# Optimization experiments

Hardware: AMD Instinct MI355X
Metric: run time of the kernel (lower is better)

Reference implementation:

```python
import jax, jax.numpy as jnp
import numpy as np

NX, NY = 8192, 8192
FX, FY = 1024, 1024
EMB, EMB_OUT = 512, 512


def setup_inputs() -> dict:
    key = jax.random.key(0)
    ks = jax.random.split(key, 8)
    s = lambda f: 1.0 / np.sqrt(f)
    return {
        "x": jax.random.normal(ks[0], (NX, FX), jnp.float32),
        "y": jax.random.normal(ks[1], (NY, FY), jnp.float32),
        "Wx": jax.random.uniform(ks[2], (FX, EMB), jnp.float32, -s(FX), s(FX)),
        "bx": jax.random.uniform(ks[3], (EMB,), jnp.float32, -s(FX), s(FX)),
        "Wy": jax.random.uniform(ks[4], (FY, EMB), jnp.float32, -s(FY), s(FY)),
        "by": jax.random.uniform(ks[5], (EMB,), jnp.float32, -s(FY), s(FY)),
        "Wg": jax.random.uniform(ks[6], (EMB, EMB_OUT), jnp.float32, -s(EMB), s(EMB)),
        "bg": jax.random.uniform(ks[7], (EMB_OUT,), jnp.float32, -s(EMB), s(EMB)),
    }


def reference(x, y, Wx, bx, Wy, by, Wg, bg):
    # Linear projections: [Nx, emb], [Ny, emb]
    xp = x @ Wx + bx
    yp = y @ Wy + by
    # Pairwise affinity (Dice-coefficient style normalization)
    A_ = xp @ yp.T                              # [Nx, Ny]
    Dcol = jnp.sum(xp * xp, axis=1)[:, None]    # ||x_i||^2, diag of xp@xp.T
    Drow = jnp.sum(yp * yp, axis=1)[None, :]    # ||y_j||^2, diag of yp@yp.T
    A = 2.0 * A_ / (Dcol + Drow)                # [Nx, Ny]
    # Weighted aggregation over x nodes, then ReLU MLP
    gwf = A.T @ xp                              # [Ny, emb]
    return jax.nn.relu(gwf @ Wg + bg)           # [Ny, emb_out]
```

## Files before the change

### kernel.cpp

```cpp
#include <hip/hip_runtime.h>
#include <hip/hip_bf16.h>


typedef __attribute__((ext_vector_type(8))) short bf16x8;
typedef __attribute__((ext_vector_type(4))) short bf16x4;
typedef __attribute__((ext_vector_type(4))) float f32x4;

__device__ __forceinline__ short f2b(float f) {
    unsigned int u = __builtin_bit_cast(unsigned int, f);
    unsigned int r = (u + 0x7fffu + ((u >> 16) & 1u)) >> 16;
    return (short)r;
}
__device__ __forceinline__ float b2f(short s) {
    unsigned int u = ((unsigned int)(unsigned short)s) << 16;
    return __builtin_bit_cast(float, u);
}

__device__ __forceinline__ void cp16(const void* g, void* l) {
    __builtin_amdgcn_global_load_lds(
        (const __attribute__((address_space(1))) void*)g,
        (__attribute__((address_space(3))) void*)l, 16, 0, 0);
}

template<int N>
__device__ __forceinline__ void waitvm() {
    if constexpr (N == 0)      asm volatile("s_waitcnt vmcnt(0)" ::: "memory");
    else if constexpr (N == 4) asm volatile("s_waitcnt vmcnt(4)" ::: "memory");
    else if constexpr (N == 6) asm volatile("s_waitcnt vmcnt(6)" ::: "memory");
    else if constexpr (N == 8) asm volatile("s_waitcnt vmcnt(8)" ::: "memory");
    else static_assert(N == 0, "unsupported vmcnt literal");
}

constexpr int EPI_XP = 0;
constexpr int EPI_BF = 1;
constexpr int EPI_AT = 2;

template<int EPI, int TM, int TN, int WVN>
__device__ __forceinline__ void gemm_core(
    const short* __restrict__ A, int lda,
    const short* __restrict__ Bt, int ldb,
    int N, int K, int bm, int bn, int kbase,
    const float* __restrict__ bias,
    short* __restrict__ outb,
    float* __restrict__ Dacc,
    const float* __restrict__ Drow, const float* __restrict__ Dcol)
{
    constexpr int WN  = WVN;
    constexpr int WM  = 4 / WN;
    constexpr int FRN = TN / WN / 16;
    constexpr int FRM = TM / WM / 16;
    __shared__ __align__(16) short As[TM * 32];
    __shared__ __align__(16) short Bs[TN * 32];

    const int tid  = threadIdx.x;
    const int wave = tid >> 6;
    const int lane = tid & 63;
    const int quad = lane >> 4;
    const int l15  = lane & 15;
    const int wn   = (wave % WN) * (FRN * 16);
    const int wm   = (wave / WN) * (FRM * 16);

    f32x4 acc[FRM][FRN];
#pragma unroll
    for (int i = 0; i < FRM; i++)
#pragma unroll
        for (int j = 0; j < FRN; j++) acc[i][j] = f32x4{0.f, 0.f, 0.f, 0.f};

    for (int k0 = kbase; k0 < kbase + K; k0 += 32) {
#pragma unroll
        for (int s = 0; s < TM / 64; s++) {
            const int seg = tid + 256 * s;
            const int row = seg >> 2, c8 = seg & 3;
            const int gg  = c8 ^ (row & 3);
            cp16(&A[(size_t)(bm + row) * lda + k0 + gg * 8], &As[seg * 8]);
        }
#pragma unroll
        for (int s = 0; s < TN / 64; s++) {
            const int seg = tid + 256 * s;
            const int row = seg >> 2, c8 = seg & 3;
            const int gg  = c8 ^ (row & 3);
            cp16(&Bt[(size_t)(bn + row) * ldb + k0 + gg * 8], &Bs[seg * 8]);
        }
        __syncthreads();

        bf16x8 a[FRM], b[FRN];
#pragma unroll
        for (int i = 0; i < FRM; i++) {
            const int row = wm + i * 16 + l15;
            a[i] = *(const bf16x8*)&As[row * 32 + ((quad ^ (row & 3)) << 3)];
        }
#pragma unroll
        for (int j = 0; j < FRN; j++) {
            const int row = wn + j * 16 + l15;
            b[j] = *(const bf16x8*)&Bs[row * 32 + ((quad ^ (row & 3)) << 3)];
        }
#pragma unroll
        for (int i = 0; i < FRM; i++)
#pragma unroll
            for (int j = 0; j < FRN; j++)
                acc[i][j] = __builtin_amdgcn_mfma_f32_16x16x32_bf16(a[i], b[j], acc[i][j], 0, 0, 0);
        __syncthreads();
    }

#pragma unroll
    for (int im = 0; im < FRM; ++im) {
#pragma unroll
        for (int r = 0; r < 4; ++r) {
            const int gm = bm + wm + im * 16 + quad * 4 + r;
            if (EPI == EPI_XP) {
                float s = 0.f;
#pragma unroll
                for (int jn = 0; jn < FRN; ++jn) {
                    const int gn = bn + wn + jn * 16 + l15;
                    const float v = acc[im][jn][r] + bias[gn];
                    outb[(size_t)gm * N + gn] = f2b(v);
                    s += v * v;
                }
#pragma unroll
                for (int m = 1; m < 16; m <<= 1) s += __shfl_xor(s, m, 64);
                if (l15 == 0) atomicAdd(&Dacc[gm], s);
            } else {
#pragma unroll
                for (int jn = 0; jn < FRN; ++jn) {
                    const int gn = bn + wn + jn * 16 + l15;
                    outb[(size_t)gm * N + gn] = f2b(acc[im][jn][r]);
                }
            }
        }
    }
}

template<int EPI, int TM, int TN, int RING>
__device__ __forceinline__ void gemm_deep(
    const short* __restrict__ A, int lda,
    const short* __restrict__ Bt, int ldb,
    int N, int K, int bm, int bn, int kbase,
    short* __restrict__ outb,
    const float* __restrict__ Drow, const float* __restrict__ Dcol)
{
    constexpr int FRM = TM / 32;
    constexpr int FRN = TN / 32;
    constexpr int CPA = TM * 4 / 256;
    constexpr int CPB = TN * 4 / 256;
    constexpr int CPT = CPA + CPB;
    __shared__ __align__(16) short As[RING][TM * 32];
    __shared__ __align__(16) short Bs[RING][TN * 32];

    const int tid  = threadIdx.x;
    const int wave = tid >> 6;
    const int lane = tid & 63;
    const int quad = lane >> 4;
    const int l15  = lane & 15;
    const int wm   = (wave >> 1) * (FRM * 16);
    const int wn   = (wave & 1) * (FRN * 16);
    const int nk   = K / 32;

    f32x4 acc[FRM][FRN];
#pragma unroll
    for (int i = 0; i < FRM; i++)
#pragma unroll
        for (int j = 0; j < FRN; j++) acc[i][j] = f32x4{0.f, 0.f, 0.f, 0.f};

    auto stage = [&](int slot, int t) {
        const int k0 = kbase + t * 32;
#pragma unroll
        for (int s = 0; s < CPA; s++) {
            const int seg = tid + 256 * s;
            const int row = seg >> 2, c8 = seg & 3;
            const int gg  = c8 ^ (row & 3);
            cp16(&A[(size_t)(bm + row) * lda + k0 + gg * 8], &As[slot][seg * 8]);
        }
#pragma unroll
        for (int s = 0; s < CPB; s++) {
            const int seg = tid + 256 * s;
            const int row = seg >> 2, c8 = seg & 3;
            const int gg  = c8 ^ (row & 3);
            cp16(&Bt[(size_t)(bn + row) * ldb + k0 + gg * 8], &Bs[slot][seg * 8]);
        }
    };

#pragma unroll
    for (int p = 0; p < RING - 1; ++p) stage(p, p);

    int cur = 0, prv = RING - 1;
    for (int t = 0; t < nk; ++t) {
        if constexpr (RING == 3) {
            if (t + 1 < nk) waitvm<CPT>(); else waitvm<0>();
        } else {
            if (t + 2 < nk)      waitvm<2 * CPT>();
            else if (t + 1 < nk) waitvm<CPT>();
            else                 waitvm<0>();
        }
        __builtin_amdgcn_s_barrier();
        if (t + RING - 1 < nk) stage(prv, t + RING - 1);

        bf16x8 a[FRM], b[FRN];
#pragma unroll
        for (int i = 0; i < FRM; i++) {
            const int row = wm + i * 16 + l15;
            a[i] = *(const bf16x8*)&As[cur][row * 32 + ((quad ^ (row & 3)) << 3)];
        }
#pragma unroll
        for (int j = 0; j < FRN; j++) {
            const int row = wn + j * 16 + l15;
            b[j] = *(const bf16x8*)&Bs[cur][row * 32 + ((quad ^ (row & 3)) << 3)];
        }
        __builtin_amdgcn_s_setprio(1);
#pragma unroll
        for (int i = 0; i < FRM; i++)
#pragma unroll
            for (int j = 0; j < FRN; j++)
                acc[i][j] = __builtin_amdgcn_mfma_f32_16x16x32_bf16(a[i], b[j], acc[i][j], 0, 0, 0);
        __builtin_amdgcn_s_setprio(0);
        asm volatile("s_waitcnt lgkmcnt(0)" ::: "memory");
        prv = cur;
        cur = (cur + 1 == RING) ? 0 : cur + 1;
    }

    if (EPI == EPI_AT) {
        float dcol[FRN];
#pragma unroll
        for (int jn = 0; jn < FRN; ++jn) dcol[jn] = Dcol[bn + wn + jn * 16 + l15];
#pragma unroll
        for (int im = 0; im < FRM; ++im) {
#pragma unroll
            for (int r = 0; r < 4; ++r) {
                const int gm = bm + wm + im * 16 + quad * 4 + r;
                const float dy = Drow[gm];
#pragma unroll
                for (int jn = 0; jn < FRN; ++jn) {
                    const int gn = bn + wn + jn * 16 + l15;
                    const float v = 2.f * acc[im][jn][r] * __builtin_amdgcn_rcpf(dcol[jn] + dy);
                    outb[(size_t)gm * N + gn] = f2b(v);
                }
            }
        }
    } else {
#pragma unroll
        for (int im = 0; im < FRM; ++im) {
#pragma unroll
            for (int r = 0; r < 4; ++r) {
                const int gm = bm + wm + im * 16 + quad * 4 + r;
#pragma unroll
                for (int jn = 0; jn < FRN; ++jn) {
                    const int gn = bn + wn + jn * 16 + l15;
                    outb[(size_t)gm * N + gn] = f2b(acc[im][jn][r]);
                }
            }
        }
    }
}

__global__ __launch_bounds__(256)
void k_proj(const short* __restrict__ A, const short* __restrict__ Bt,
            const float* __restrict__ bias, short* __restrict__ outb,
            float* __restrict__ Dacc)
{
    gemm_core<EPI_XP, 64, 128, 2>(A, 1024, Bt, 1024, 512, 1024,
                                  blockIdx.y * 64, blockIdx.x * 128, 0,
                                  bias, outb, Dacc, nullptr, nullptr);
}

__global__ __launch_bounds__(256)
void k_zT(const short* __restrict__ WgT, const short* __restrict__ xpb,
          short* __restrict__ zT)
{
    gemm_core<EPI_BF, 64, 128, 2>(WgT, 512, xpb, 512, 8192, 512,
                                  blockIdx.y * 64, blockIdx.x * 128, 0,
                                  nullptr, zT, nullptr, nullptr, nullptr);
}

__global__ __launch_bounds__(256, 2)
void k_aff(const short* __restrict__ ypb, const short* __restrict__ xpb,
           short* __restrict__ At, const float* __restrict__ Dy,
           const float* __restrict__ Dx)
{
    const int flat = blockIdx.x;
    const int xcd = flat & 7;
    const int q   = flat >> 3;
    const int by  = xcd * 4 + (q & 3);
    const int bx  = q >> 2;
    gemm_deep<EPI_AT, 256, 128, 3>(ypb, 512, xpb, 512, 8192, 512,
                                   by * 256, bx * 128, 0, At, Dy, Dx);
}

__global__ __launch_bounds__(256, 2)
void k_agg(const short* __restrict__ At, const short* __restrict__ zT,
           short* __restrict__ p0, short* __restrict__ p1)
{
    const int flat = blockIdx.x;
    const int xcd = flat & 7;
    const int q   = flat >> 3;
    const int g   = xcd * 16 + (q >> 2);
    const int bm  = (g >> 1) * 128;
    const int z   = g & 1;
    const int bn  = (q & 3) * 128;
    short* outb = z ? p1 : p0;
    gemm_deep<EPI_BF, 128, 128, 4>(At, 8192, zT, 8192, 512, 4096,
                                   bm, bn, z * 4096, outb, nullptr, nullptr);
}

__global__ __launch_bounds__(256)
void k_fin(const short* __restrict__ p0, const short* __restrict__ p1,
           const float* __restrict__ bg, float* __restrict__ out)
{
    const int idx = (blockIdx.x * 256 + threadIdx.x) * 8;
    const int col = idx & 511;
    const bf16x8 a = *(const bf16x8*)&p0[idx];
    const bf16x8 b = *(const bf16x8*)&p1[idx];
    const f32x4 g0 = *(const f32x4*)&bg[col];
    const f32x4 g1 = *(const f32x4*)&bg[col + 4];
    f32x4 o0, o1;
#pragma unroll
    for (int e = 0; e < 4; ++e) {
        o0[e] = fmaxf(b2f(a[e]) + b2f(b[e]) + g0[e], 0.f);
        o1[e] = fmaxf(b2f(a[e + 4]) + b2f(b[e + 4]) + g1[e], 0.f);
    }
    *(f32x4*)&out[idx]     = o0;
    *(f32x4*)&out[idx + 4] = o1;
}

__global__ __launch_bounds__(256)
void k_cvt(const float* __restrict__ in, short* __restrict__ out)
{
    const int i = (blockIdx.x * 256 + threadIdx.x) * 4;
    const float4 v = *(const float4*)&in[i];
    bf16x4 b;
    b[0] = f2b(v.x); b[1] = f2b(v.y); b[2] = f2b(v.z); b[3] = f2b(v.w);
    *(bf16x4*)&out[i] = b;
}

__global__ __launch_bounds__(256)
void transpose_f32_bf16(const float* __restrict__ in, short* __restrict__ out, int R, int C)
{
    __shared__ short t[32][33];
    const int tx = threadIdx.x, ty = threadIdx.y;
    const int bx = blockIdx.x * 32, by = blockIdx.y * 32;
#pragma unroll
    for (int i = 0; i < 32; i += 8)
        t[ty + i][tx] = f2b(in[(size_t)(by + ty + i) * C + bx + tx]);
    __syncthreads();
#pragma unroll
    for (int i = 0; i < 32; i += 8)
        out[(size_t)(bx + ty + i) * R + by + tx] = t[tx][ty + i];
}

extern "C" void kernel_launch(void* const* d_in, const int* in_sizes, int n_in,
                              void* d_out, int out_size, void* d_ws, size_t ws_size,
                              hipStream_t stream)
{
    const float* x  = (const float*)d_in[0];
    const float* y  = (const float*)d_in[1];
    const float* Wx = (const float*)d_in[2];
    const float* bx = (const float*)d_in[3];
    const float* Wy = (const float*)d_in[4];
    const float* by = (const float*)d_in[5];
    const float* Wg = (const float*)d_in[6];
    const float* bg = (const float*)d_in[7];
    float* out = (float*)d_out;

    char* p = (char*)d_ws;
    short* At   = (short*)p;
    short* xb   = (short*)p;
    short* yb   = (short*)(p + (size_t)8192 * 1024 * 2);
    p += (size_t)8192 * 8192 * 2;
    short* xpb  = (short*)p; p += (size_t)8192 * 512 * 2;
    short* ypb  = (short*)p; p += (size_t)8192 * 512 * 2;
    short* zT   = (short*)p; p += (size_t)512 * 8192 * 2;
    short* WxT  = (short*)p; p += (size_t)512 * 1024 * 2;
    short* WyT  = (short*)p; p += (size_t)512 * 1024 * 2;
    short* WgT  = (short*)p; p += (size_t)512 * 512 * 2;
    float* Dx   = (float*)p; p += (size_t)8192 * 4;
    float* Dy   = (float*)p; p += (size_t)8192 * 4;
    short* p0 = xpb;
    short* p1 = ypb;

    hipMemsetAsync(Dx, 0, 2 * 8192 * sizeof(float), stream);

    dim3 tb(32, 8);
    transpose_f32_bf16<<<dim3(512 / 32, 1024 / 32), tb, 0, stream>>>(Wx, WxT, 1024, 512);
    transpose_f32_bf16<<<dim3(512 / 32, 1024 / 32), tb, 0, stream>>>(Wy, WyT, 1024, 512);
    transpose_f32_bf16<<<dim3(512 / 32, 512 / 32),  tb, 0, stream>>>(Wg, WgT, 512, 512);

    k_cvt<<<8192, 256, 0, stream>>>(x, xb);
    k_cvt<<<8192, 256, 0, stream>>>(y, yb);

    k_proj<<<dim3(4, 128), 256, 0, stream>>>(xb, WxT, bx, xpb, Dx);
    k_proj<<<dim3(4, 128), 256, 0, stream>>>(yb, WyT, by, ypb, Dy);

    k_zT<<<dim3(64, 8), 256, 0, stream>>>(WgT, xpb, zT);

    k_aff<<<2048, 256, 0, stream>>>(ypb, xpb, At, Dy, Dx);

    k_agg<<<512, 256, 0, stream>>>(At, zT, p0, p1);

    k_fin<<<2048, 256, 0, stream>>>(p0, p1, bg, out);
}
```

Measured before the change: 356.1 us.

## Load B fragments directly from global into registers in deep GEMM

The deep GEMM no longer stages the B operand through LDS. Each wave now loads its own B fragments straight from global memory into registers and prefetches the next k-step one iteration ahead, and the vmcnt waits are adjusted to count these loads. This cuts LDS footprint and LDS traffic for B and frees LDS for occupancy, at the cost of less-coalesced global loads and duplicated B reads across waves that share columns. It also removes unused Drow/Dcol parameters from gemm_core.

```diff
diff --git a/kernel.cpp b/kernel.cpp
--- a/kernel.cpp
+++ b/kernel.cpp
@@ -24,10 +24,14 @@
 
 template<int N>
 __device__ __forceinline__ void waitvm() {
-    if constexpr (N == 0)      asm volatile("s_waitcnt vmcnt(0)" ::: "memory");
-    else if constexpr (N == 4) asm volatile("s_waitcnt vmcnt(4)" ::: "memory");
-    else if constexpr (N == 6) asm volatile("s_waitcnt vmcnt(6)" ::: "memory");
-    else if constexpr (N == 8) asm volatile("s_waitcnt vmcnt(8)" ::: "memory");
+    if constexpr (N == 0)       asm volatile("s_waitcnt vmcnt(0)" ::: "memory");
+    else if constexpr (N == 2)  asm volatile("s_waitcnt vmcnt(2)" ::: "memory");
+    else if constexpr (N == 4)  asm volatile("s_waitcnt vmcnt(4)" ::: "memory");
+    else if constexpr (N == 6)  asm volatile("s_waitcnt vmcnt(6)" ::: "memory");
+    else if constexpr (N == 8)  asm volatile("s_waitcnt vmcnt(8)" ::: "memory");
+    else if constexpr (N == 10) asm volatile("s_waitcnt vmcnt(10)" ::: "memory");
+    else if constexpr (N == 12) asm volatile("s_waitcnt vmcnt(12)" ::: "memory");
+    else if constexpr (N == 16) asm volatile("s_waitcnt vmcnt(16)" ::: "memory");
     else static_assert(N == 0, "unsupported vmcnt literal");
 }
 
@@ -42,8 +46,7 @@
     int N, int K, int bm, int bn, int kbase,
     const float* __restrict__ bias,
     short* __restrict__ outb,
-    float* __restrict__ Dacc,
-    const float* __restrict__ Drow, const float* __restrict__ Dcol)
+    float* __restrict__ Dacc)
 {
     constexpr int WN  = WVN;
     constexpr int WM  = 4 / WN;
@@ -141,10 +144,8 @@
     constexpr int FRM = TM / 32;
     constexpr int FRN = TN / 32;
     constexpr int CPA = TM * 4 / 256;
-    constexpr int CPB = TN * 4 / 256;
-    constexpr int CPT = CPA + CPB;
+    constexpr int FB  = FRN;
     __shared__ __align__(16) short As[RING][TM * 32];
-    __shared__ __align__(16) short Bs[RING][TN * 32];
 
     const int tid  = threadIdx.x;
     const int wave = tid >> 6;
@@ -155,13 +156,18 @@
     const int wn   = (wave & 1) * (FRN * 16);
     const int nk   = K / 32;
 
+    const short* bp[FRN];
+#pragma unroll
+    for (int j = 0; j < FRN; j++)
+        bp[j] = Bt + (size_t)(bn + wn + j * 16 + l15) * ldb + kbase + quad * 8;
+
     f32x4 acc[FRM][FRN];
 #pragma unroll
     for (int i = 0; i < FRM; i++)
 #pragma unroll
         for (int j = 0; j < FRN; j++) acc[i][j] = f32x4{0.f, 0.f, 0.f, 0.f};
 
-    auto stage = [&](int slot, int t) {
+    auto stageA = [&](int slot, int t) {
         const int k0 = kbase + t * 32;
 #pragma unroll
         for (int s = 0; s < CPA; s++) {
@@ -170,49 +176,50 @@
             const int gg  = c8 ^ (row & 3);
             cp16(&A[(size_t)(bm + row) * lda + k0 + gg * 8], &As[slot][seg * 8]);
         }
-#pragma unroll
-        for (int s = 0; s < CPB; s++) {
-            const int seg = tid + 256 * s;
-            const int row = seg >> 2, c8 = seg & 3;
-            const int gg  = c8 ^ (row & 3);
-            cp16(&Bt[(size_t)(bn + row) * ldb + k0 + gg * 8], &Bs[slot][seg * 8]);
-        }
     };
 
 #pragma unroll
-    for (int p = 0; p < RING - 1; ++p) stage(p, p);
+    for (int p = 0; p < RING - 1; ++p) stageA(p, p);
+    bf16x8 bc[FRN], bnx[FRN];
+#pragma unroll
+    for (int j = 0; j < FRN; j++) bc[j] = *(const bf16x8*)(bp[j]);
 
     int cur = 0, prv = RING - 1;
     for (int t = 0; t < nk; ++t) {
         if constexpr (RING == 3) {
-            if (t + 1 < nk) waitvm<CPT>(); else waitvm<0>();
+            if (t + 1 < nk) waitvm<CPA + FB>();
+            else            waitvm<0>();
         } else {
-            if (t + 2 < nk)      waitvm<2 * CPT>();
-            else if (t + 1 < nk) waitvm<CPT>();
+            if (t + 2 < nk)      waitvm<2 * (CPA + FB)>();
+            else if (t + 1 < nk) waitvm<CPA + FB>();
             else                 waitvm<0>();
         }
         __builtin_amdgcn_s_barrier();
-        if (t + RING - 1 < nk) stage(prv, t + RING - 1);
-
-        bf16x8 a[FRM], b[FRN];
+        if (t + 1 < nk) {
+#pragma unroll
+            for (int j = 0; j < FRN; j++)
+                bnx[j] = *(const bf16x8*)(bp[j] + (size_t)(t + 1) * 32);
+        }
+        if (t + RING - 1 < nk) stageA(prv, t + RING - 1);
+
+        bf16x8 a[FRM];
 #pragma unroll
         for (int i = 0; i < FRM; i++) {
             const int row = wm + i * 16 + l15;
             a[i] = *(const bf16x8*)&As[cur][row * 32 + ((quad ^ (row & 3)) << 3)];
         }
-#pragma unroll
-        for (int j = 0; j < FRN; j++) {
-            const int row = wn + j * 16 + l15;
-            b[j] = *(const bf16x8*)&Bs[cur][row * 32 + ((quad ^ (row & 3)) << 3)];
-        }
         __builtin_amdgcn_s_setprio(1);
 #pragma unroll
         for (int i = 0; i < FRM; i++)
 #pragma unroll
             for (int j = 0; j < FRN; j++)
-                acc[i][j] = __builtin_amdgcn_mfma_f32_16x16x32_bf16(a[i], b[j], acc[i][j], 0, 0, 0);
+                acc[i][j] = __builtin_amdgcn_mfma_f32_16x16x32_bf16(a[i], bc[j], acc[i][j], 0, 0, 0);
         __builtin_amdgcn_s_setprio(0);
         asm volatile("s_waitcnt lgkmcnt(0)" ::: "memory");
+        if (t + 1 < nk) {
+#pragma unroll
+            for (int j = 0; j < FRN; j++) bc[j] = bnx[j];
+        }
         prv = cur;
         cur = (cur + 1 == RING) ? 0 : cur + 1;
     }
@@ -258,7 +265,7 @@
 {
     gemm_core<EPI_XP, 64, 128, 2>(A, 1024, Bt, 1024, 512, 1024,
                                   blockIdx.y * 64, blockIdx.x * 128, 0,
-                                  bias, outb, Dacc, nullptr, nullptr);
+                                  bias, outb, Dacc);
 }
 
 __global__ __launch_bounds__(256)
@@ -267,7 +274,7 @@
 {
     gemm_core<EPI_BF, 64, 128, 2>(WgT, 512, xpb, 512, 8192, 512,
                                   blockIdx.y * 64, blockIdx.x * 128, 0,
-                                  nullptr, zT, nullptr, nullptr, nullptr);
+                                  nullptr, zT, nullptr);
 }
 
 __global__ __launch_bounds__(256, 2)
```

Result: slower. 427.8 us (+20.1%).
